# Performance work log

Measured on AMD Instinct MI355X. Metric: run time of the kernel, lower is better.

The kernel has to match this reference:

```python
import jax, jax.numpy as jnp
import numpy as np

D_K = 64

def setup_inputs() -> dict:
    key = jax.random.key(0)
    k1, k2, k3, k4 = jax.random.split(key, 4)
    hidden_states = jax.random.normal(k1, (2, 16, 128, 16, 16), dtype=jnp.float32)
    # nn.Linear(hidden, d, bias=False); stored as [in, out] for x @ W
    w_q = jax.random.normal(k2, (128, 64), dtype=jnp.float32) * 0.05
    w_k = jax.random.normal(k3, (128, 64), dtype=jnp.float32) * 0.05
    w_v = jax.random.normal(k4, (128, 64), dtype=jnp.float32) * 0.05
    return {"hidden_states": hidden_states, "w_q": w_q, "w_k": w_k, "w_v": w_v}

def reference(hidden_states, w_q, w_k, w_v):
    # (B, T, C, H, W) -> (B, T, H, W, C) -> (N, C)
    x = jnp.transpose(hidden_states, (0, 1, 3, 4, 2))
    x = x.reshape(-1, x.shape[-1])                      # [N, C], N = B*T*H*W
    q = x @ w_q                                          # [N, d_k]
    k = x @ w_k                                          # [N, d_k]
    v = x @ w_v                                          # [N, d_v]
    scores = (q @ k.T) / jnp.sqrt(jnp.asarray(D_K, x.dtype))  # [N, N]
    attn = jax.nn.softmax(scores, axis=1)                # softmax over dim=1
    out = attn @ v                                       # [N, d_v]
    return out
```

## Files before the change

kernel.cpp:

```cpp
#include <hip/hip_runtime.h>
#include <hip/hip_bf16.h>

typedef float f32x4 __attribute__((ext_vector_type(4)));
typedef short bf16x8 __attribute__((ext_vector_type(8)));
typedef short bf16x4 __attribute__((ext_vector_type(4)));

#define MFMA32 __builtin_amdgcn_mfma_f32_16x16x32_bf16

#if __has_builtin(__builtin_amdgcn_mfma_f32_16x16x16bf16_1k)
#define HAVE_MFMA16 1
#else
#define HAVE_MFMA16 0
#endif

__device__ __forceinline__ unsigned short f2bf(float f) {
  union { float f; unsigned u; } v; v.f = f;
  unsigned u = v.u;
  u += 0x7FFFu + ((u >> 16) & 1u);
  return (unsigned short)(u >> 16);
}

__device__ __forceinline__ bf16x4 pack4_bf16(float a, float b, float c, float d) {
  union { bf16x4 v; __hip_bfloat162 h[2]; } u;
  u.h[0] = __float22bfloat162_rn(make_float2(a, b));
  u.h[1] = __float22bfloat162_rn(make_float2(c, d));
  return u.v;
}

__device__ __forceinline__ f32x4 pv_mfma(bf16x4 av, bf16x4 pf, f32x4 acc) {
#if HAVE_MFMA16
  return __builtin_amdgcn_mfma_f32_16x16x16bf16_1k(av, pf, acc, 0, 0, 0);
#else
  bf16x8 a8 = {av[0], av[1], av[2], av[3], 0, 0, 0, 0};
  bf16x8 b8 = {pf[0], pf[1], pf[2], pf[3], 0, 0, 0, 0};
  return MFMA32(a8, b8, acc, 0, 0, 0);
#endif
}

__global__ __launch_bounds__(256) void qkv_kernel(
    const float* __restrict__ hs,
    const float* __restrict__ wq, const float* __restrict__ wk,
    const float* __restrict__ wv,
    unsigned short* __restrict__ qb, unsigned short* __restrict__ kpack,
    unsigned short* __restrict__ vpack)
{
  __shared__ __align__(16) float Wl[128 * 64];
  __shared__ float xs[32 * 129];
  const int t = threadIdx.x;
  const int mat = blockIdx.y;
  const float* __restrict__ W = (mat == 0) ? wq : (mat == 1) ? wk : wv;
  #pragma unroll
  for (int i = 0; i < 8; ++i) {
    *(f32x4*)(Wl + i * 1024 + t * 4) = *(const f32x4*)(W + i * 1024 + t * 4);
  }
  const int n0 = blockIdx.x * 32;
  const int bt = n0 >> 8;
  const int sp0 = n0 & 255;
  {
    const float* __restrict__ src = hs + (size_t)bt * 32768 + sp0;
    const int s = t & 31, cb = t >> 5;
    #pragma unroll
    for (int i = 0; i < 16; ++i) {
      const int c = i * 8 + cb;
      xs[s * 129 + c] = src[c * 256 + s];
    }
  }
  __syncthreads();
  const int s = t & 31, g = t >> 5;
  float acc[8];
  #pragma unroll
  for (int j = 0; j < 8; ++j) acc[j] = 0.f;
  #pragma unroll 4
  for (int c = 0; c < 128; ++c) {
    const float xv = xs[s * 129 + c];
    const f32x4 w0 = *(const f32x4*)(Wl + c * 64 + g * 8);
    const f32x4 w1 = *(const f32x4*)(Wl + c * 64 + g * 8 + 4);
    acc[0] += xv * w0[0]; acc[1] += xv * w0[1];
    acc[2] += xv * w0[2]; acc[3] += xv * w0[3];
    acc[4] += xv * w1[0]; acc[5] += xv * w1[1];
    acc[6] += xv * w1[2]; acc[7] += xv * w1[3];
  }
  const int n = n0 + s;
  const float SCALE = 1.4426950408889634f / 8.0f;
  if (mat == 0) {
    #pragma unroll
    for (int j = 0; j < 8; ++j) qb[n * 64 + g * 8 + j] = f2bf(acc[j] * SCALE);
  } else if (mat == 1) {
    const int kvb = n >> 4, low16 = n & 15;
    const int h = g >> 2, quadk = g & 3;
    unsigned short* dst = kpack + ((size_t)(kvb * 2 + h) * 64 + quadk * 16 + low16) * 8;
    #pragma unroll
    for (int j = 0; j < 8; ++j) dst[j] = f2bf(acc[j]);
  } else {
    const int kvb = n >> 4, quadv = (n >> 2) & 3, ii = n & 3;
    #pragma unroll
    for (int j = 0; j < 8; ++j) {
      const int d = g * 8 + j, dt = d >> 4, lowd = d & 15;
      vpack[((size_t)(kvb * 4 + dt) * 64 + quadv * 16 + lowd) * 4 + ii] = f2bf(acc[j]);
    }
  }
}

__global__ __launch_bounds__(256, 4) void flash_kernel(
    const unsigned short* __restrict__ qb,
    const unsigned short* __restrict__ kpack,
    const unsigned short* __restrict__ vpack,
    float* __restrict__ opart, float* __restrict__ lpart, int kvlen)
{
  const int t = threadIdx.x;
  const int w = t >> 6, lane = t & 63;
  const int quad = lane >> 4, low = lane & 15;
  const int bid = blockIdx.x;
  const int q0 = (bid & 63) * 128 + w * 32;
  const int g = bid >> 6;
  const int kvb0 = (g * kvlen) >> 4;
  const int nIter = kvlen >> 4;

  bf16x8 bq[2][2];
  #pragma unroll
  for (int qt = 0; qt < 2; ++qt)
    #pragma unroll
    for (int h = 0; h < 2; ++h)
      bq[qt][h] = *(const bf16x8*)(qb + (q0 + qt * 16 + low) * 64 + h * 32 + quad * 8);

  f32x4 O[2][4];
  float lac[2] = {0.f, 0.f};
  #pragma unroll
  for (int qt = 0; qt < 2; ++qt)
    #pragma unroll
    for (int dt = 0; dt < 4; ++dt) O[qt][dt] = (f32x4){0.f, 0.f, 0.f, 0.f};

  const unsigned short* kp = kpack + (size_t)kvb0 * 1024 + lane * 8;
  const unsigned short* vp = vpack + (size_t)kvb0 * 1024 + lane * 4;

  bf16x8 akc0 = *(const bf16x8*)(kp);
  bf16x8 akc1 = *(const bf16x8*)(kp + 512);
  bf16x4 avc[4];
  #pragma unroll
  for (int dt = 0; dt < 4; ++dt) avc[dt] = *(const bf16x4*)(vp + dt * 256);

  #pragma unroll 2
  for (int it = 0; it < nIter; ++it) {
    const int nx = (it + 1 < nIter) ? it + 1 : it;
    const unsigned short* kpn = kp + (size_t)nx * 1024;
    const unsigned short* vpn = vp + (size_t)nx * 1024;
    const bf16x8 akn0 = *(const bf16x8*)(kpn);
    const bf16x8 akn1 = *(const bf16x8*)(kpn + 512);
    bf16x4 avn[4];
    #pragma unroll
    for (int dt = 0; dt < 4; ++dt) avn[dt] = *(const bf16x4*)(vpn + dt * 256);

    #pragma unroll
    for (int qt = 0; qt < 2; ++qt) {
      f32x4 S = {0.f, 0.f, 0.f, 0.f};
      S = MFMA32(akc0, bq[qt][0], S, 0, 0, 0);
      S = MFMA32(akc1, bq[qt][1], S, 0, 0, 0);
      const float p0 = __builtin_amdgcn_exp2f(S[0]);
      const float p1 = __builtin_amdgcn_exp2f(S[1]);
      const float p2 = __builtin_amdgcn_exp2f(S[2]);
      const float p3 = __builtin_amdgcn_exp2f(S[3]);
      lac[qt] += (p0 + p1) + (p2 + p3);
      const bf16x4 pf = pack4_bf16(p0, p1, p2, p3);
      #pragma unroll
      for (int dt = 0; dt < 4; ++dt)
        O[qt][dt] = pv_mfma(avc[dt], pf, O[qt][dt]);
    }
    akc0 = akn0; akc1 = akn1;
    #pragma unroll
    for (int dt = 0; dt < 4; ++dt) avc[dt] = avn[dt];
  }

  #pragma unroll
  for (int qt = 0; qt < 2; ++qt) {
    const size_t qrow = (size_t)g * 8192 + q0 + qt * 16;
    #pragma unroll
    for (int dt = 0; dt < 4; ++dt)
      *(f32x4*)(opart + (qrow + low) * 64 + dt * 16 + quad * 4) = O[qt][dt];
    float l = lac[qt];
    l += __shfl_xor(l, 16);
    l += __shfl_xor(l, 32);
    if (quad == 0) lpart[qrow + low] = l;
  }
}

__global__ __launch_bounds__(256) void reduce_kernel(
    const float* __restrict__ opart, const float* __restrict__ lpart,
    float* __restrict__ out, int G)
{
  const int idx = blockIdx.x * 256 + threadIdx.x;
  const int q = idx >> 6;
  const int d = idx & 63;
  float num = 0.f, den = 0.f;
  for (int g = 0; g < G; ++g) {
    den += lpart[g * 8192 + q];
    num += opart[((size_t)g * 8192 + q) * 64 + d];
  }
  out[idx] = num / den;
}

extern "C" void kernel_launch(void* const* d_in, const int* in_sizes, int n_in,
                              void* d_out, int out_size, void* d_ws, size_t ws_size,
                              hipStream_t stream) {
  const float* hs = (const float*)d_in[0];
  const float* wq = (const float*)d_in[1];
  const float* wk = (const float*)d_in[2];
  const float* wv = (const float*)d_in[3];
  float* out = (float*)d_out;
  char* ws = (char*)d_ws;

  unsigned short* qb    = (unsigned short*)ws;
  unsigned short* kpack = (unsigned short*)(ws + (1 << 20));
  unsigned short* vpack = (unsigned short*)(ws + (2 << 20));

  int G = 16;
  {
    const size_t per_g = (size_t)8192 * 64 * 4 + (size_t)8192 * 4;
    while (G > 1 && ws_size < (size_t)(3 << 20) + (size_t)G * per_g) G >>= 1;
  }
  float* opart = (float*)(ws + (3 << 20));
  float* lpart = (float*)(ws + (3 << 20) + (size_t)G * 8192 * 64 * 4);

  qkv_kernel<<<dim3(256, 3, 1), 256, 0, stream>>>(hs, wq, wk, wv, qb, kpack, vpack);
  flash_kernel<<<64 * G, 256, 0, stream>>>(qb, kpack, vpack, opart, lpart, 8192 / G);
  reduce_kernel<<<2048, 256, 0, stream>>>(opart, lpart, out, G);
}
```

Measured before the change: 118.9 us.

## Widen per-wave query tile, deepen KV prefetch, double split-K, vectorize reduce

Each wave now handles 64 query rows instead of 32, so every K/V fragment loaded from global memory feeds twice as many MFMAs. The K/V register prefetch becomes two iterations deep to hide load latency, and occupancy drops from 4 to 3 blocks per CU to leave room for the extra registers. The KV dimension is split into 32 groups instead of 16, which keeps the block count the same but doubles the partial output buffer the reduce pass must read. The reduce kernel now reads and writes float4 vectors and multiplies by a reciprocal instead of dividing.

```diff
diff --git a/kernel.cpp b/kernel.cpp
--- a/kernel.cpp
+++ b/kernel.cpp
@@ -101,7 +101,7 @@
   }
 }
 
-__global__ __launch_bounds__(256, 4) void flash_kernel(
+__global__ __launch_bounds__(256, 3) void flash_kernel(
     const unsigned short* __restrict__ qb,
     const unsigned short* __restrict__ kpack,
     const unsigned short* __restrict__ vpack,
@@ -111,50 +111,55 @@
   const int w = t >> 6, lane = t & 63;
   const int quad = lane >> 4, low = lane & 15;
   const int bid = blockIdx.x;
-  const int q0 = (bid & 63) * 128 + w * 32;
-  const int g = bid >> 6;
+  const int q0 = (bid & 31) * 256 + w * 64;
+  const int g = bid >> 5;
   const int kvb0 = (g * kvlen) >> 4;
   const int nIter = kvlen >> 4;
 
-  bf16x8 bq[2][2];
-  #pragma unroll
-  for (int qt = 0; qt < 2; ++qt)
+  bf16x8 bq[4][2];
+  #pragma unroll
+  for (int qt = 0; qt < 4; ++qt)
     #pragma unroll
     for (int h = 0; h < 2; ++h)
       bq[qt][h] = *(const bf16x8*)(qb + (q0 + qt * 16 + low) * 64 + h * 32 + quad * 8);
 
-  f32x4 O[2][4];
-  float lac[2] = {0.f, 0.f};
-  #pragma unroll
-  for (int qt = 0; qt < 2; ++qt)
+  f32x4 O[4][4];
+  float lac[4] = {0.f, 0.f, 0.f, 0.f};
+  #pragma unroll
+  for (int qt = 0; qt < 4; ++qt)
     #pragma unroll
     for (int dt = 0; dt < 4; ++dt) O[qt][dt] = (f32x4){0.f, 0.f, 0.f, 0.f};
 
   const unsigned short* kp = kpack + (size_t)kvb0 * 1024 + lane * 8;
   const unsigned short* vp = vpack + (size_t)kvb0 * 1024 + lane * 4;
 
-  bf16x8 akc0 = *(const bf16x8*)(kp);
-  bf16x8 akc1 = *(const bf16x8*)(kp + 512);
-  bf16x4 avc[4];
-  #pragma unroll
-  for (int dt = 0; dt < 4; ++dt) avc[dt] = *(const bf16x4*)(vp + dt * 256);
-
-  #pragma unroll 2
+  bf16x8 k0[2], k1[2], k2[2];
+  bf16x4 v0[4], v1[4], v2[4];
+  k0[0] = *(const bf16x8*)(kp);
+  k0[1] = *(const bf16x8*)(kp + 512);
+  #pragma unroll
+  for (int dt = 0; dt < 4; ++dt) v0[dt] = *(const bf16x4*)(vp + dt * 256);
+  const int i1 = (nIter > 1) ? 1 : 0;
+  k1[0] = *(const bf16x8*)(kp + (size_t)i1 * 1024);
+  k1[1] = *(const bf16x8*)(kp + (size_t)i1 * 1024 + 512);
+  #pragma unroll
+  for (int dt = 0; dt < 4; ++dt)
+    v1[dt] = *(const bf16x4*)(vp + (size_t)i1 * 1024 + dt * 256);
+
+  #pragma unroll 3
   for (int it = 0; it < nIter; ++it) {
-    const int nx = (it + 1 < nIter) ? it + 1 : it;
-    const unsigned short* kpn = kp + (size_t)nx * 1024;
-    const unsigned short* vpn = vp + (size_t)nx * 1024;
-    const bf16x8 akn0 = *(const bf16x8*)(kpn);
-    const bf16x8 akn1 = *(const bf16x8*)(kpn + 512);
-    bf16x4 avn[4];
-    #pragma unroll
-    for (int dt = 0; dt < 4; ++dt) avn[dt] = *(const bf16x4*)(vpn + dt * 256);
-
-    #pragma unroll
-    for (int qt = 0; qt < 2; ++qt) {
+    const int nx = (it + 2 < nIter) ? it + 2 : nIter - 1;
+    k2[0] = *(const bf16x8*)(kp + (size_t)nx * 1024);
+    k2[1] = *(const bf16x8*)(kp + (size_t)nx * 1024 + 512);
+    #pragma unroll
+    for (int dt = 0; dt < 4; ++dt)
+      v2[dt] = *(const bf16x4*)(vp + (size_t)nx * 1024 + dt * 256);
+
+    #pragma unroll
+    for (int qt = 0; qt < 4; ++qt) {
       f32x4 S = {0.f, 0.f, 0.f, 0.f};
-      S = MFMA32(akc0, bq[qt][0], S, 0, 0, 0);
-      S = MFMA32(akc1, bq[qt][1], S, 0, 0, 0);
+      S = MFMA32(k0[0], bq[qt][0], S, 0, 0, 0);
+      S = MFMA32(k0[1], bq[qt][1], S, 0, 0, 0);
       const float p0 = __builtin_amdgcn_exp2f(S[0]);
       const float p1 = __builtin_amdgcn_exp2f(S[1]);
       const float p2 = __builtin_amdgcn_exp2f(S[2]);
@@ -163,15 +168,16 @@
       const bf16x4 pf = pack4_bf16(p0, p1, p2, p3);
       #pragma unroll
       for (int dt = 0; dt < 4; ++dt)
-        O[qt][dt] = pv_mfma(avc[dt], pf, O[qt][dt]);
+        O[qt][dt] = pv_mfma(v0[dt], pf, O[qt][dt]);
     }
-    akc0 = akn0; akc1 = akn1;
-    #pragma unroll
-    for (int dt = 0; dt < 4; ++dt) avc[dt] = avn[dt];
-  }
-
-  #pragma unroll
-  for (int qt = 0; qt < 2; ++qt) {
+    k0[0] = k1[0]; k0[1] = k1[1];
+    k1[0] = k2[0]; k1[1] = k2[1];
+    #pragma unroll
+    for (int dt = 0; dt < 4; ++dt) { v0[dt] = v1[dt]; v1[dt] = v2[dt]; }
+  }
+
+  #pragma unroll
+  for (int qt = 0; qt < 4; ++qt) {
     const size_t qrow = (size_t)g * 8192 + q0 + qt * 16;
     #pragma unroll
     for (int dt = 0; dt < 4; ++dt)
@@ -188,14 +194,18 @@
     float* __restrict__ out, int G)
 {
   const int idx = blockIdx.x * 256 + threadIdx.x;
-  const int q = idx >> 6;
-  const int d = idx & 63;
-  float num = 0.f, den = 0.f;
+  const int q = idx >> 4;
+  const int d4 = (idx & 15) * 4;
+  float den = 0.f;
+  f32x4 num = {0.f, 0.f, 0.f, 0.f};
   for (int g = 0; g < G; ++g) {
     den += lpart[g * 8192 + q];
-    num += opart[((size_t)g * 8192 + q) * 64 + d];
-  }
-  out[idx] = num / den;
+    const f32x4 o = *(const f32x4*)(opart + ((size_t)g * 8192 + q) * 64 + d4);
+    num[0] += o[0]; num[1] += o[1]; num[2] += o[2]; num[3] += o[3];
+  }
+  const float r = 1.0f / den;
+  f32x4 res = {num[0] * r, num[1] * r, num[2] * r, num[3] * r};
+  *(f32x4*)(out + (size_t)q * 64 + d4) = res;
 }
 
 extern "C" void kernel_launch(void* const* d_in, const int* in_sizes, int n_in,
@@ -212,7 +222,7 @@
   unsigned short* kpack = (unsigned short*)(ws + (1 << 20));
   unsigned short* vpack = (unsigned short*)(ws + (2 << 20));
 
-  int G = 16;
+  int G = 32;
   {
     const size_t per_g = (size_t)8192 * 64 * 4 + (size_t)8192 * 4;
     while (G > 1 && ws_size < (size_t)(3 << 20) + (size_t)G * per_g) G >>= 1;
@@ -221,6 +231,6 @@
   float* lpart = (float*)(ws + (3 << 20) + (size_t)G * 8192 * 64 * 4);
 
   qkv_kernel<<<dim3(256, 3, 1), 256, 0, stream>>>(hs, wq, wk, wv, qb, kpack, vpack);
-  flash_kernel<<<64 * G, 256, 0, stream>>>(qb, kpack, vpack, opart, lpart, 8192 / G);
-  reduce_kernel<<<2048, 256, 0, stream>>>(opart, lpart, out, G);
-}
+  flash_kernel<<<32 * G, 256, 0, stream>>>(qb, kpack, vpack, opart, lpart, 8192 / G);
+  reduce_kernel<<<512, 256, 0, stream>>>(opart, lpart, out, G);
+}
```

Result: no change. 117.8 us (-0.9%).
